# Kernel optimization log

Hardware: AMD Instinct MI355X
Metric: run time of the kernel (lower is better)

Reference implementation:

```python
import jax, jax.numpy as jnp
import numpy as np

TEMPERATURE = 0.1
NEG_INF = -1e30


def setup_inputs() -> dict:
    key = jax.random.key(0)
    kf, kl = jax.random.split(key)
    N, D = 8192, 128
    features = jax.random.normal(kf, (N, D), dtype=jnp.float32)
    # labels in [-1, 80): -1 marks background rows that are filtered out
    labels = jax.random.randint(kl, (N,), -1, 80)
    return {"features": features, "labels": labels}


def reference(features, labels):
    N = labels.shape[0]
    fg = labels >= 0  # [N]

    # F.normalize(p=2, dim=1): x / max(||x||, eps)
    norm = jnp.maximum(jnp.linalg.norm(features, axis=1, keepdims=True), 1e-12)
    f = features / norm

    sim = jnp.matmul(f, f.T) / TEMPERATURE  # [N, N]

    pair_fg = fg[:, None] & fg[None, :]
    eye = jnp.eye(N, dtype=bool)
    label_eq = labels[:, None] == labels[None, :]
    pos_mask = pair_fg & label_eq & ~eye          # positives (same label, not self)
    all_mask = pair_fg & ~eye                     # pos | neg == everything but self (within fg)

    # row-wise masked max, clamped to [-20, 20] as in the original
    max_sim = jnp.max(jnp.where(all_mask, sim, NEG_INF), axis=1)
    max_sim = jnp.clip(max_sim, -20.0, 20.0)

    e = jnp.exp(sim - max_sim[:, None])           # cos-sim/temp is bounded, no overflow
    pos_sum = jnp.clip(jnp.sum(jnp.where(pos_mask, e, 0.0), axis=1), 1e-6, 1e6)
    all_sum = jnp.clip(jnp.sum(jnp.where(all_mask, e, 0.0), axis=1), 1e-6, 1e6)

    loss_i = jnp.minimum(-jnp.log(pos_sum / all_sum), 10.0)  # clamp(max=10)

    # rows contributing to the mean: fg rows with at least one positive
    valid = fg & (jnp.sum(pos_mask, axis=1) > 0)
    n_valid = jnp.sum(valid)
    mean_loss = jnp.sum(jnp.where(valid, loss_i, 0.0)) / jnp.maximum(n_valid, 1).astype(jnp.float32)

    ok = (jnp.sum(fg) >= 2) & (n_valid > 0)
    return jnp.where(ok, mean_loss, jnp.float32(0.0))
```

## Files before the change

### kernel.cpp

```cpp
#include <hip/hip_runtime.h>

#define N 8192
#define D 128
#define CHUNK 512
#define NCC (N / CHUNK)
#define NHT 8
#define NBIN 81
#define PBLK 512

typedef unsigned short u16;
typedef __attribute__((ext_vector_type(8))) __bf16 bf16x8;
typedef __attribute__((ext_vector_type(4))) float f32x4;

#define PREP_SCALE 3.7982889979f

__device__ __forceinline__ u16 f2bf(float x) {
  unsigned u = __float_as_uint(x);
  u += 0x7fff + ((u >> 16) & 1);
  return (u16)(u >> 16);
}

__global__ __launch_bounds__(256) void cpe_prep(const float* __restrict__ feat,
                                                const int* __restrict__ labels,
                                                u16* __restrict__ fhi,
                                                int* __restrict__ slab,
                                                float* __restrict__ acc3) {
  __shared__ int hist[4][NBIN], part[4][NBIN], lbase[NBIN], lpos[16];
  const int tid = threadIdx.x;
  const int w = tid >> 6, l = tid & 63;
  const int bid = blockIdx.x;
  if (tid < NBIN) {
#pragma unroll
    for (int cp = 0; cp < 4; ++cp) { hist[cp][tid] = 0; part[cp][tid] = 0; }
  }
  if (bid == 0 && tid < 4) acc3[tid] = 0.0f;
  __syncthreads();
  const int myBase = bid * 16;
  for (int j = tid; j < N; j += 256) {
    const int lab = labels[j] + 1;
    atomicAdd(&hist[w][lab], 1);
    if (j < myBase) atomicAdd(&part[w][lab], 1);
  }
  __syncthreads();
  if (tid < NBIN) {
    hist[0][tid] += hist[1][tid] + hist[2][tid] + hist[3][tid];
    part[0][tid] += part[1][tid] + part[2][tid] + part[3][tid];
  }
  __syncthreads();
  if (tid == 0) {
    int s = 0;
    for (int b = 0; b < NBIN; ++b) { lbase[b] = s; s += hist[0][b]; }
  }
  __syncthreads();
  if (tid < 16) {
    const int L = labels[myBase + tid] + 1;
    int pos = lbase[L] + part[0][L];
    for (int k = 0; k < tid; ++k) pos += (labels[myBase + k] + 1 == L) ? 1 : 0;
    lpos[tid] = pos;
    slab[pos] = L - 1;
  }
  __syncthreads();
#pragma unroll
  for (int rr = 0; rr < 4; ++rr) {
    const int k = w * 4 + rr;
    const float2 x = *(const float2*)&feat[(myBase + k) * D + l * 2];
    float s = x.x * x.x + x.y * x.y;
#pragma unroll
    for (int sh = 1; sh < 64; sh <<= 1) s += __shfl_xor(s, sh);
    const float inv = PREP_SCALE / fmaxf(sqrtf(s), 1e-12f);
    const int pos = lpos[k];
    *(ushort2*)&fhi[pos * D + l * 2] = make_ushort2(f2bf(x.x * inv), f2bf(x.y * inv));
  }
}

__global__ __launch_bounds__(256, 2) void cpe_main(
    const u16* __restrict__ fhi, const int* __restrict__ slab,
    float2* __restrict__ partials) {
  __shared__ __align__(16) u16 Bh[2][64 * 128];
  __shared__ int Lab[CHUNK];
  const int rt = blockIdx.x, cc = blockIdx.y;
  const int tid = threadIdx.x;
  const int w = tid >> 6, l = tid & 63, q = l >> 4, m = l & 15;
  const int r0w = rt * 256 + w * 64;
  const int cbase0 = cc * CHUNK;

#define STAGE(buf, ht)                                                         \
  do {                                                                         \
    const int cb_ = cbase0 + (ht) * 64;                                        \
    _Pragma("unroll") for (int n = 0; n < 4; ++n) {                            \
      const int r_ = w * 16 + n * 4 + q;                                       \
      const int c_ = m ^ (r_ & 15);                                            \
      const u16* gh_ = &fhi[(size_t)(cb_ + r_) * D + c_ * 8];                  \
      __builtin_amdgcn_global_load_lds(                                        \
          (const __attribute__((address_space(1))) unsigned*)gh_,              \
          (__attribute__((address_space(3))) unsigned*)&Bh[buf][(w * 256 + n * 64) * 8], \
          16, 0, 0);                                                           \
    }                                                                          \
  } while (0)

  STAGE(0, 0);

  Lab[tid] = slab[cbase0 + tid];
  Lab[tid + 256] = slab[cbase0 + 256 + tid];

  const int labi_lo = slab[r0w], labi_hi = slab[r0w + 63];

  bf16x8 Ah[4][4];
  int labi[4][4];
#pragma unroll
  for (int tr = 0; tr < 4; ++tr) {
    const int row = r0w + tr * 16 + m;
#pragma unroll
    for (int ks = 0; ks < 4; ++ks)
      Ah[tr][ks] = *(const bf16x8*)&fhi[row * D + ks * 32 + q * 8];
#pragma unroll
    for (int v = 0; v < 4; ++v) labi[tr][v] = slab[r0w + tr * 16 + q * 4 + v];
  }

  float ps[4][4], as_[4][4];
#pragma unroll
  for (int tr = 0; tr < 4; ++tr)
#pragma unroll
    for (int v = 0; v < 4; ++v) { ps[tr][v] = 0.f; as_[tr][v] = 0.f; }

  __syncthreads();

  for (int ht = 0; ht < NHT; ++ht) {
    const int cur = ht & 1;
    if (ht + 1 < NHT) STAGE(cur ^ 1, ht + 1);

    for (int ct = 0; ct < 4; ++ct) {
      const int tb = ht * 64 + ct * 16;
      const int labj_lo = Lab[tb], labj_hi = Lab[tb + 15];
      if (labj_hi < 0) continue;
      const bool slow = (labj_lo < 0) | ((labj_hi >= labi_lo) & (labj_lo <= labi_hi));
      const int jj = ct * 16 + m;
      f32x4 acc[4];
#pragma unroll
      for (int tr = 0; tr < 4; ++tr) acc[tr] = (f32x4){0.f, 0.f, 0.f, 0.f};
#pragma unroll
      for (int ks = 0; ks < 4; ++ks) {
        const int off = jj * 128 + ((ks * 4 + q) ^ m) * 8;
        const bf16x8 bh = *(const bf16x8*)&Bh[cur][off];
#pragma unroll
        for (int tr = 0; tr < 4; ++tr)
          acc[tr] = __builtin_amdgcn_mfma_f32_16x16x32_bf16(Ah[tr][ks], bh, acc[tr], 0, 0, 0);
      }
      if (!slow) {
#pragma unroll
        for (int tr = 0; tr < 4; ++tr)
#pragma unroll
          for (int v = 0; v < 4; ++v)
            as_[tr][v] += __builtin_amdgcn_exp2f(acc[tr][v]);
      } else {
        const int labj = Lab[tb + m];
        const bool fgj = labj >= 0;
        const int jbase = cbase0 + tb;
#pragma unroll
        for (int tr = 0; tr < 4; ++tr) {
          if (jbase == r0w + tr * 16) {
#pragma unroll
            for (int v = 0; v < 4; ++v) {
              const float e = __builtin_amdgcn_exp2f(acc[tr][v]);
              const float em = (fgj && (m != q * 4 + v)) ? e : 0.0f;
              as_[tr][v] += em;
              ps[tr][v] += (labj == labi[tr][v]) ? em : 0.0f;
            }
          } else {
#pragma unroll
            for (int v = 0; v < 4; ++v) {
              const float e = __builtin_amdgcn_exp2f(acc[tr][v]);
              const float em = fgj ? e : 0.0f;
              as_[tr][v] += em;
              ps[tr][v] += (labj == labi[tr][v]) ? em : 0.0f;
            }
          }
        }
      }
    }
    __syncthreads();
  }
#undef STAGE

#pragma unroll
  for (int tr = 0; tr < 4; ++tr)
#pragma unroll
    for (int v = 0; v < 4; ++v) {
      float vp = ps[tr][v], va = as_[tr][v];
#pragma unroll
      for (int s = 1; s < 16; s <<= 1) {
        vp += __shfl_xor(vp, s);
        va += __shfl_xor(va, s);
      }
      if (m == 0)
        partials[(size_t)cc * N + r0w + tr * 16 + q * 4 + v] = make_float2(vp, va);
    }
}

__global__ __launch_bounds__(256) void cpe_rows(const float2* __restrict__ partials,
                                                const int* __restrict__ slab,
                                                float* __restrict__ acc3,
                                                float* __restrict__ out) {
  const int r = blockIdx.x * 256 + threadIdx.x;
  float psr = 0.f, asr = 0.f;
#pragma unroll
  for (int c = 0; c < NCC; ++c) {
    const float2 p = partials[(size_t)c * N + r];
    psr += p.x;
    asr += p.y;
  }
  const bool fg = slab[r] >= 0;
  const bool valid = fg && (psr > 0.f);
  const float loss = fminf(logf(asr / psr), 10.0f);
  float v0 = valid ? loss : 0.f;
  float v1 = valid ? 1.f : 0.f;
  float v2 = fg ? 1.f : 0.f;
#pragma unroll
  for (int s = 1; s < 64; s <<= 1) {
    v0 += __shfl_xor(v0, s);
    v1 += __shfl_xor(v1, s);
    v2 += __shfl_xor(v2, s);
  }
  __shared__ float red[3][4];
  const int w = threadIdx.x >> 6, l = threadIdx.x & 63;
  if (l == 0) { red[0][w] = v0; red[1][w] = v1; red[2][w] = v2; }
  __syncthreads();
  if (threadIdx.x == 0) {
    atomicAdd(&acc3[0], red[0][0] + red[0][1] + red[0][2] + red[0][3]);
    atomicAdd(&acc3[1], red[1][0] + red[1][1] + red[1][2] + red[1][3]);
    atomicAdd(&acc3[2], red[2][0] + red[2][1] + red[2][2] + red[2][3]);
    __threadfence();
    const unsigned old = atomicAdd((unsigned*)&acc3[3], 1u);
    if (old == gridDim.x - 1) {
      const float ls = atomicAdd(&acc3[0], 0.0f);
      const float nv = atomicAdd(&acc3[1], 0.0f);
      const float nf = atomicAdd(&acc3[2], 0.0f);
      out[0] = (nf >= 2.0f && nv > 0.0f) ? ls / fmaxf(nv, 1.0f) : 0.0f;
    }
  }
}

extern "C" void kernel_launch(void* const* d_in, const int* in_sizes, int n_in,
                              void* d_out, int out_size, void* d_ws, size_t ws_size,
                              hipStream_t stream) {
  const float* feat = (const float*)d_in[0];
  const int* labels = (const int*)d_in[1];
  float* out = (float*)d_out;
  char* ws = (char*)d_ws;
  u16* fhi = (u16*)ws;
  float2* partials = (float2*)(ws + (size_t)N * D * 2);
  char* tail = ws + (size_t)N * D * 2 + (size_t)NCC * N * 8;
  int* slab = (int*)tail;
  float* acc3 = (float*)(tail + N * 4);

  cpe_prep<<<PBLK, 256, 0, stream>>>(feat, labels, fhi, slab, acc3);
  cpe_main<<<dim3(N / 256, NCC), 256, 0, stream>>>(fhi, slab, partials);
  cpe_rows<<<N / 256, 256, 0, stream>>>(partials, slab, acc3, out);
}
```

Baseline: 103.3 us.

## Exploit similarity symmetry by computing only upper-triangular tiles with column partials

Because the similarity matrix is symmetric, the main kernel now processes only the upper-triangular block tiles (256-row by 128-column chunks, launched as a 1D triangular grid). Each tile accumulates row sums as before and also column sums, which are reduced through shared memory and written to a second partials buffer. The row-finalize kernel combines the row partials and the transposed column partials. This roughly halves the MFMA and exp work, but adds column reductions, shuffles and shared-memory traffic, and gives an uneven triangular mapping of blocks.

```diff
diff --git a/kernel.cpp b/kernel.cpp
--- a/kernel.cpp
+++ b/kernel.cpp
@@ -2,9 +2,10 @@
 
 #define N 8192
 #define D 128
-#define CHUNK 512
-#define NCC (N / CHUNK)
-#define NHT 8
+#define RCH 256
+#define CCH 128
+#define NRC (N / RCH)
+#define NCCH (N / CCH)
 #define NBIN 81
 #define PBLK 512
 
@@ -75,14 +76,18 @@
 
 __global__ __launch_bounds__(256, 2) void cpe_main(
     const u16* __restrict__ fhi, const int* __restrict__ slab,
-    float2* __restrict__ partials) {
+    float2* __restrict__ partA, float2* __restrict__ partB) {
   __shared__ __align__(16) u16 Bh[2][64 * 128];
-  __shared__ int Lab[CHUNK];
-  const int rt = blockIdx.x, cc = blockIdx.y;
+  __shared__ int Lab[CCH];
+  __shared__ float LcA[4][CCH], LcP[4][CCH];
   const int tid = threadIdx.x;
   const int w = tid >> 6, l = tid & 63, q = l >> 4, m = l & 15;
-  const int r0w = rt * 256 + w * 64;
-  const int cbase0 = cc * CHUNK;
+
+  int b = blockIdx.x, rt = 0;
+  while (b >= NCCH - 2 * rt) { b -= NCCH - 2 * rt; ++rt; }
+  const int cc = 2 * rt + b;
+  const int r0 = rt * RCH, cbase0 = cc * CCH;
+  const int r0w = r0 + w * 64;
 
 #define STAGE(buf, ht)                                                         \
   do {                                                                         \
@@ -100,8 +105,7 @@
 
   STAGE(0, 0);
 
-  Lab[tid] = slab[cbase0 + tid];
-  Lab[tid + 256] = slab[cbase0 + 256 + tid];
+  if (tid < CCH) Lab[tid] = slab[cbase0 + tid];
 
   const int labi_lo = slab[r0w], labi_hi = slab[r0w + 63];
 
@@ -122,60 +126,82 @@
   for (int tr = 0; tr < 4; ++tr)
 #pragma unroll
     for (int v = 0; v < 4; ++v) { ps[tr][v] = 0.f; as_[tr][v] = 0.f; }
-
-  __syncthreads();
-
-  for (int ht = 0; ht < NHT; ++ht) {
-    const int cur = ht & 1;
-    if (ht + 1 < NHT) STAGE(cur ^ 1, ht + 1);
-
-    for (int ct = 0; ct < 4; ++ct) {
-      const int tb = ht * 64 + ct * 16;
+  float csA0 = 0.f, csA1 = 0.f, csP0 = 0.f, csP1 = 0.f;
+
+  __syncthreads();
+
+#pragma unroll
+  for (int ht = 0; ht < 2; ++ht) {
+    if (ht == 0) STAGE(1, 1);
+
+#pragma unroll
+    for (int ctl = 0; ctl < 4; ++ctl) {
+      const int tct = ht * 4 + ctl;
+      const int tb = tct * 16;
+      const int jbase = cbase0 + tb;
       const int labj_lo = Lab[tb], labj_hi = Lab[tb + 15];
-      if (labj_hi < 0) continue;
-      const bool slow = (labj_lo < 0) | ((labj_hi >= labi_lo) & (labj_lo <= labi_hi));
-      const int jj = ct * 16 + m;
+      if (labj_hi < 0 || jbase < r0w) continue;
+
       f32x4 acc[4];
 #pragma unroll
       for (int tr = 0; tr < 4; ++tr) acc[tr] = (f32x4){0.f, 0.f, 0.f, 0.f};
 #pragma unroll
       for (int ks = 0; ks < 4; ++ks) {
-        const int off = jj * 128 + ((ks * 4 + q) ^ m) * 8;
-        const bf16x8 bh = *(const bf16x8*)&Bh[cur][off];
+        const int off = (ctl * 16 + m) * 128 + ((ks * 4 + q) ^ m) * 8;
+        const bf16x8 bh = *(const bf16x8*)&Bh[ht][off];
 #pragma unroll
         for (int tr = 0; tr < 4; ++tr)
           acc[tr] = __builtin_amdgcn_mfma_f32_16x16x32_bf16(Ah[tr][ks], bh, acc[tr], 0, 0, 0);
       }
+
+      float cAs = 0.f, cPs = 0.f;
+      const bool slow = (labj_lo < 0) | ((labj_hi >= labi_lo) & (labj_lo <= labi_hi));
       if (!slow) {
 #pragma unroll
-        for (int tr = 0; tr < 4; ++tr)
-#pragma unroll
-          for (int v = 0; v < 4; ++v)
-            as_[tr][v] += __builtin_amdgcn_exp2f(acc[tr][v]);
+        for (int tr = 0; tr < 4; ++tr) {
+          if (jbase > r0w + tr * 16) {
+#pragma unroll
+            for (int v = 0; v < 4; ++v) {
+              const float e = __builtin_amdgcn_exp2f(acc[tr][v]);
+              as_[tr][v] += e;
+              cAs += (labi[tr][v] >= 0) ? e : 0.f;
+            }
+          }
+        }
       } else {
         const int labj = Lab[tb + m];
         const bool fgj = labj >= 0;
-        const int jbase = cbase0 + tb;
 #pragma unroll
         for (int tr = 0; tr < 4; ++tr) {
-          if (jbase == r0w + tr * 16) {
+          const int rowbase = r0w + tr * 16;
+          if (jbase > rowbase) {
 #pragma unroll
             for (int v = 0; v < 4; ++v) {
               const float e = __builtin_amdgcn_exp2f(acc[tr][v]);
-              const float em = (fgj && (m != q * 4 + v)) ? e : 0.0f;
+              const bool eq = (labj == labi[tr][v]);
+              const float em = fgj ? e : 0.f;
               as_[tr][v] += em;
-              ps[tr][v] += (labj == labi[tr][v]) ? em : 0.0f;
+              ps[tr][v] += eq ? em : 0.f;
+              const float emc = (labi[tr][v] >= 0) ? e : 0.f;
+              cAs += emc;
+              cPs += eq ? emc : 0.f;
             }
-          } else {
+          } else if (jbase == rowbase) {
 #pragma unroll
             for (int v = 0; v < 4; ++v) {
               const float e = __builtin_amdgcn_exp2f(acc[tr][v]);
-              const float em = fgj ? e : 0.0f;
+              const float em = (fgj && (m != q * 4 + v)) ? e : 0.f;
               as_[tr][v] += em;
-              ps[tr][v] += (labj == labi[tr][v]) ? em : 0.0f;
+              ps[tr][v] += (labj == labi[tr][v]) ? em : 0.f;
             }
           }
         }
+      }
+      cAs += __shfl_xor(cAs, 16); cAs += __shfl_xor(cAs, 32);
+      cPs += __shfl_xor(cPs, 16); cPs += __shfl_xor(cPs, 32);
+      if ((tct >> 1) == q) {
+        if ((tct & 1) == 0) { csA0 = cAs; csP0 = cPs; }
+        else               { csA1 = cAs; csP1 = cPs; }
       }
     }
     __syncthreads();
@@ -193,21 +219,36 @@
         va += __shfl_xor(va, s);
       }
       if (m == 0)
-        partials[(size_t)cc * N + r0w + tr * 16 + q * 4 + v] = make_float2(vp, va);
+        partA[(size_t)cc * N + r0w + tr * 16 + q * 4 + v] = make_float2(vp, va);
     }
-}
-
-__global__ __launch_bounds__(256) void cpe_rows(const float2* __restrict__ partials,
+
+  LcA[w][(q * 2 + 0) * 16 + m] = csA0;
+  LcA[w][(q * 2 + 1) * 16 + m] = csA1;
+  LcP[w][(q * 2 + 0) * 16 + m] = csP0;
+  LcP[w][(q * 2 + 1) * 16 + m] = csP1;
+  __syncthreads();
+  if (tid < CCH) {
+    const float a = LcA[0][tid] + LcA[1][tid] + LcA[2][tid] + LcA[3][tid];
+    const float p = LcP[0][tid] + LcP[1][tid] + LcP[2][tid] + LcP[3][tid];
+    partB[(size_t)rt * N + cbase0 + tid] = make_float2(p, a);
+  }
+}
+
+__global__ __launch_bounds__(256) void cpe_rows(const float2* __restrict__ partA,
+                                                const float2* __restrict__ partB,
                                                 const int* __restrict__ slab,
                                                 float* __restrict__ acc3,
                                                 float* __restrict__ out) {
-  const int r = blockIdx.x * 256 + threadIdx.x;
+  const int rtb = blockIdx.x;
+  const int r = rtb * 256 + threadIdx.x;
   float psr = 0.f, asr = 0.f;
-#pragma unroll
-  for (int c = 0; c < NCC; ++c) {
-    const float2 p = partials[(size_t)c * N + r];
-    psr += p.x;
-    asr += p.y;
+  for (int k = 2 * rtb; k < NCCH; ++k) {
+    const float2 p = partA[(size_t)k * N + r];
+    psr += p.x; asr += p.y;
+  }
+  for (int t = 0; t <= rtb; ++t) {
+    const float2 p = partB[(size_t)t * N + r];
+    psr += p.x; asr += p.y;
   }
   const bool fg = slab[r] >= 0;
   const bool valid = fg && (psr > 0.f);
@@ -248,12 +289,14 @@
   float* out = (float*)d_out;
   char* ws = (char*)d_ws;
   u16* fhi = (u16*)ws;
-  float2* partials = (float2*)(ws + (size_t)N * D * 2);
-  char* tail = ws + (size_t)N * D * 2 + (size_t)NCC * N * 8;
+  float2* partA = (float2*)(ws + (size_t)N * D * 2);
+  float2* partB = (float2*)(ws + (size_t)N * D * 2 + (size_t)NCCH * N * 8);
+  char* tail = ws + (size_t)N * D * 2 + (size_t)(NCCH + NRC) * N * 8;
   int* slab = (int*)tail;
   float* acc3 = (float*)(tail + N * 4);
 
+  const int nblk = 1056;
   cpe_prep<<<PBLK, 256, 0, stream>>>(feat, labels, fhi, slab, acc3);
-  cpe_main<<<dim3(N / 256, NCC), 256, 0, stream>>>(fhi, slab, partials);
-  cpe_rows<<<N / 256, 256, 0, stream>>>(partials, slab, acc3, out);
-}
+  cpe_main<<<nblk, 256, 0, stream>>>(fhi, slab, partA, partB);
+  cpe_rows<<<NRC, 256, 0, stream>>>(partA, partB, slab, acc3, out);
+}
```

Result: slower. 118.7 us (+14.9%).
